# Optimization experiments

Measured on AMD Instinct MI355X. Metric: run time of the kernel, lower is better.

Reference implementation:

```python
import jax, jax.numpy as jnp
import numpy as np

S, N, F, DEG, D_IN, D_OUT = 8, 50000, 5, 32, 128, 128


def setup_inputs() -> dict:
    key = jax.random.key(0)
    k1, k2, k3, k4, k5 = jax.random.split(key, 5)
    std = 1.0 / np.sqrt(D_OUT)
    x = jax.random.normal(k1, (S, N, F), dtype=jnp.float32)
    neigh_idx = jax.random.randint(k2, (S, N, DEG), 0, N, dtype=jnp.int32)
    W_1 = jax.random.uniform(k3, (F, D_IN), minval=-std, maxval=std, dtype=jnp.float32)
    W = jax.random.uniform(k4, (2 * D_IN, D_OUT), minval=-std, maxval=std, dtype=jnp.float32)
    b = jax.random.uniform(k5, (D_OUT,), minval=-std, maxval=std, dtype=jnp.float32)
    return {"x": x, "neigh_idx": neigh_idx, "W_1": W_1, "W": W, "b": b}


def reference(x, neigh_idx, W_1, W, b):
    # Self features projected through W_1 (the x_ list in the torch code).
    self_feats = jnp.einsum('snf,fd->snd', x, W_1)          # [S, N, D_IN]
    # Aggregator: mean over sampled neighbors' raw features (per sample).
    gathered = jax.vmap(lambda xs, ids: xs[ids])(x, neigh_idx)  # [S, N, DEG, F]
    neigh_raw = gathered.mean(axis=2)                        # [S, N, F]
    neigh_feats = jnp.einsum('snf,fd->snd', neigh_raw, W_1)  # [S, N, D_IN]
    # combine == 'concat'
    combined = jnp.concatenate([self_feats, neigh_feats], axis=-1)  # [S, N, 2*D_IN]
    y = jnp.einsum('snc,co->sno', combined, W) + b           # [S, N, D_OUT]
    return jax.nn.relu(y)
```

## Files before the change

### kernel.cpp

```cpp
#include <hip/hip_runtime.h>
#include <cstddef>
#include <cstdint>

static constexpr int S_    = 8;
static constexpr int N_    = 50000;
static constexpr int F_    = 5;
static constexpr int DEG_  = 32;
static constexpr int DOUT_ = 128;
static constexpr int TOTAL_NODES = S_ * N_;
static constexpr int NODES_PER_WAVE = 8;
static constexpr int GROUPS = TOTAL_NODES / NODES_PER_WAVE;

typedef float    f32x4 __attribute__((ext_vector_type(4)));
typedef int      i32x4 __attribute__((ext_vector_type(4)));
typedef _Float16 h2    __attribute__((ext_vector_type(2)));

__global__ void wc_precompute(const float* __restrict__ W1,
                              const float* __restrict__ W,
                              float* __restrict__ Wc) {
    int t = blockIdx.x * blockDim.x + threadIdx.x;
    if (t >= 2 * F_ * DOUT_) return;
    int o = t & (DOUT_ - 1);
    int f = (t >> 7) % F_;
    int p = t / (F_ * DOUT_);
    const float* w1r  = W1 + f * 128;
    const float* wcol = W + (size_t)p * 128 * DOUT_ + o;
    float acc = 0.f;
#pragma unroll 8
    for (int d = 0; d < 128; ++d)
        acc = fmaf(w1r[d], wcol[(size_t)d * DOUT_], acc);
    Wc[t] = acc;
}

struct alignas(16) H8 { _Float16 v[8]; };

__global__ __launch_bounds__(256) void xpack_f16(const float* __restrict__ x,
                                                 H8* __restrict__ xh) {
    int t = blockIdx.x * blockDim.x + threadIdx.x;
    if (t >= TOTAL_NODES) return;
    const float* r = x + (size_t)t * F_;
    H8 o;
#pragma unroll
    for (int f = 0; f < F_; ++f) o.v[f] = (_Float16)r[f];
#pragma unroll
    for (int f = F_; f < 8; ++f) o.v[f] = (_Float16)0.f;
    xh[t] = o;
}

__global__ __launch_bounds__(256) void encoder_v3(
    const int*   __restrict__ idx,
    const H8*    __restrict__ xh,
    const float* __restrict__ Wc,
    const float* __restrict__ b,
    float* __restrict__ out) {
    const int lane = threadIdx.x & 63;
    const int sl   = lane & 31;
    const int half = lane >> 5;
    const int o0   = sl << 2;
    const int g    = (blockIdx.x * blockDim.x + threadIdx.x) >> 6;

    float wa[F_][4], wb[F_][4];
#pragma unroll
    for (int f = 0; f < F_; ++f) {
        f32x4 a  = *reinterpret_cast<const f32x4*>(Wc + f * DOUT_ + o0);
        f32x4 bb = *reinterpret_cast<const f32x4*>(Wc + F_ * DOUT_ + f * DOUT_ + o0);
        wa[f][0] = a.x;  wa[f][1] = a.y;  wa[f][2] = a.z;  wa[f][3] = a.w;
        wb[f][0] = bb.x; wb[f][1] = bb.y; wb[f][2] = bb.z; wb[f][3] = bb.w;
    }
    const f32x4 bias = *reinterpret_cast<const f32x4*>(b + o0);
    const float inv = 1.f / DEG_;

    const int base = g * NODES_PER_WAVE;
    const int s    = base / N_;
    const H8* xs   = xh + (size_t)s * N_;

    union U { i32x4 i; h2 h[4]; };

    int node[4], nb[4];
#pragma unroll
    for (int j = 0; j < 4; ++j) {
        node[j] = base + half + 2 * j;
        nb[j] = __builtin_nontemporal_load(idx + (size_t)node[j] * DEG_ + sl);
    }
    U gv[4], sv[4];
#pragma unroll
    for (int j = 0; j < 4; ++j) {
        gv[j].i = *reinterpret_cast<const i32x4*>(xs + nb[j]);
        sv[j].i = *reinterpret_cast<const i32x4*>(xh + node[j]);
    }

#pragma unroll
    for (int j = 0; j < 4; ++j) {
        h2 v0 = gv[j].h[0], v1 = gv[j].h[1], v2 = gv[j].h[2];
#pragma unroll
        for (int m = 1; m < 32; m <<= 1) {
            v0 += __builtin_bit_cast(h2, __shfl_xor(__builtin_bit_cast(int, v0), m));
            v1 += __builtin_bit_cast(h2, __shfl_xor(__builtin_bit_cast(int, v1), m));
            v2 += __builtin_bit_cast(h2, __shfl_xor(__builtin_bit_cast(int, v2), m));
        }
        const float nf[F_] = { (float)v0.x * inv, (float)v0.y * inv,
                               (float)v1.x * inv, (float)v1.y * inv,
                               (float)v2.x * inv };
        const float sf[F_] = { (float)sv[j].h[0].x, (float)sv[j].h[0].y,
                               (float)sv[j].h[1].x, (float)sv[j].h[1].y,
                               (float)sv[j].h[2].x };
        float y0 = bias.x, y1 = bias.y, y2 = bias.z, y3 = bias.w;
#pragma unroll
        for (int f = 0; f < F_; ++f) {
            y0 = fmaf(sf[f], wa[f][0], y0); y0 = fmaf(nf[f], wb[f][0], y0);
            y1 = fmaf(sf[f], wa[f][1], y1); y1 = fmaf(nf[f], wb[f][1], y1);
            y2 = fmaf(sf[f], wa[f][2], y2); y2 = fmaf(nf[f], wb[f][2], y2);
            y3 = fmaf(sf[f], wa[f][3], y3); y3 = fmaf(nf[f], wb[f][3], y3);
        }
        f32x4 yv = { fmaxf(y0, 0.f), fmaxf(y1, 0.f), fmaxf(y2, 0.f), fmaxf(y3, 0.f) };
        __builtin_nontemporal_store(yv,
            reinterpret_cast<f32x4*>(out + (size_t)node[j] * DOUT_ + o0));
    }
}

__global__ __launch_bounds__(256) void encoder_f32(
    const float* __restrict__ x, const int* __restrict__ idx,
    const float* __restrict__ Wc, const float* __restrict__ b,
    float* __restrict__ out, int total_pairs) {
    const int lane = threadIdx.x & 63;
    const int sl   = lane & 31;
    const int half = lane >> 5;
    const int o0   = sl << 2;
    const int gwave  = (blockIdx.x * blockDim.x + threadIdx.x) >> 6;
    const int nwaves = (gridDim.x * blockDim.x) >> 6;
    float wa[F_][4], wb[F_][4];
#pragma unroll
    for (int f = 0; f < F_; ++f) {
        f32x4 a  = *reinterpret_cast<const f32x4*>(Wc + f * DOUT_ + o0);
        f32x4 bb = *reinterpret_cast<const f32x4*>(Wc + F_ * DOUT_ + f * DOUT_ + o0);
        wa[f][0] = a.x;  wa[f][1] = a.y;  wa[f][2] = a.z;  wa[f][3] = a.w;
        wb[f][0] = bb.x; wb[f][1] = bb.y; wb[f][2] = bb.z; wb[f][3] = bb.w;
    }
    const f32x4 bias = *reinterpret_cast<const f32x4*>(b + o0);
    for (int p = gwave; p < total_pairs; p += nwaves) {
        const int node = p * 2 + half;
        const int s    = node / N_;
        const int nb = idx[(size_t)node * DEG_ + sl];
        const float* xr = x + ((size_t)s * N_ + nb) * F_;
        float n0 = xr[0], n1 = xr[1], n2 = xr[2], n3 = xr[3], n4 = xr[4];
#pragma unroll
        for (int m = 1; m < 32; m <<= 1) {
            n0 += __shfl_xor(n0, m); n1 += __shfl_xor(n1, m); n2 += __shfl_xor(n2, m);
            n3 += __shfl_xor(n3, m); n4 += __shfl_xor(n4, m);
        }
        const float inv = 1.f / DEG_;
        const float nf[F_] = {n0 * inv, n1 * inv, n2 * inv, n3 * inv, n4 * inv};
        const float* xsp = x + (size_t)node * F_;
        const float sf[F_] = {xsp[0], xsp[1], xsp[2], xsp[3], xsp[4]};
        float y0 = bias.x, y1 = bias.y, y2 = bias.z, y3 = bias.w;
#pragma unroll
        for (int f = 0; f < F_; ++f) {
            y0 = fmaf(sf[f], wa[f][0], y0); y0 = fmaf(nf[f], wb[f][0], y0);
            y1 = fmaf(sf[f], wa[f][1], y1); y1 = fmaf(nf[f], wb[f][1], y1);
            y2 = fmaf(sf[f], wa[f][2], y2); y2 = fmaf(nf[f], wb[f][2], y2);
            y3 = fmaf(sf[f], wa[f][3], y3); y3 = fmaf(nf[f], wb[f][3], y3);
        }
        f32x4 yv = { fmaxf(y0, 0.f), fmaxf(y1, 0.f), fmaxf(y2, 0.f), fmaxf(y3, 0.f) };
        *reinterpret_cast<f32x4*>(out + (size_t)node * DOUT_ + o0) = yv;
    }
}

extern "C" void kernel_launch(void* const* d_in, const int* in_sizes, int n_in,
                              void* d_out, int out_size, void* d_ws, size_t ws_size,
                              hipStream_t stream) {
    const float* x   = (const float*)d_in[0];
    const int*   idx = (const int*)  d_in[1];
    const float* W1  = (const float*)d_in[2];
    const float* W   = (const float*)d_in[3];
    const float* b   = (const float*)d_in[4];
    float* out = (float*)d_out;

    const size_t wc_bytes = (size_t)2 * F_ * DOUT_ * sizeof(float);
    const size_t xh_bytes = (size_t)TOTAL_NODES * sizeof(H8);
    float* Wc = (float*)d_ws;

    hipLaunchKernelGGL(wc_precompute, dim3(5), dim3(256), 0, stream, W1, W, Wc);

    if (ws_size >= wc_bytes + xh_bytes) {
        H8* xh = (H8*)((char*)d_ws + wc_bytes);
        hipLaunchKernelGGL(xpack_f16, dim3((TOTAL_NODES + 255) / 256), dim3(256),
                           0, stream, x, xh);
        hipLaunchKernelGGL(encoder_v3, dim3(GROUPS / 4), dim3(256), 0, stream,
                           idx, xh, Wc, b, out);
    } else {
        hipLaunchKernelGGL(encoder_f32, dim3(2048), dim3(256), 0, stream,
                           x, idx, Wc, b, out, S_ * N_ / 2);
    }
}
```

Before: 129.0 us.

## Pack neighbor features to fp8 and software-pipeline a persistent encoder loop

Neighbor features are now packed to fp8, 8 bytes per node, instead of fp16 in 16 bytes, which halves the random-gather footprint. Self features are read in full fp32 directly from x. The encoder becomes persistent: 4096 waves each process a contiguous range of groups. A double-buffered loop prefetches indices and gathered features for the next groups while computing the current one, to hide gather latency. The risk is lower accuracy from fp8 neighbor features, plus extra register pressure from the double buffers.

```diff
diff --git a/kernel.cpp b/kernel.cpp
--- a/kernel.cpp
+++ b/kernel.cpp
@@ -8,11 +8,14 @@
 static constexpr int DEG_  = 32;
 static constexpr int DOUT_ = 128;
 static constexpr int TOTAL_NODES = S_ * N_;
-static constexpr int NODES_PER_WAVE = 8;
-static constexpr int GROUPS = TOTAL_NODES / NODES_PER_WAVE;
+static constexpr int NODES_PER_GROUP = 8;
+static constexpr int GROUPS = TOTAL_NODES / NODES_PER_GROUP;
+static constexpr int NWAVES = 4096;
+static constexpr int KLO    = GROUPS / NWAVES;
+static constexpr int RHI    = GROUPS - KLO * NWAVES;
 
 typedef float    f32x4 __attribute__((ext_vector_type(4)));
-typedef int      i32x4 __attribute__((ext_vector_type(4)));
+typedef int      i32x2 __attribute__((ext_vector_type(2)));
 typedef _Float16 h2    __attribute__((ext_vector_type(2)));
 
 __global__ void wc_precompute(const float* __restrict__ W1,
@@ -32,24 +35,78 @@
     Wc[t] = acc;
 }
 
-struct alignas(16) H8 { _Float16 v[8]; };
-
-__global__ __launch_bounds__(256) void xpack_f16(const float* __restrict__ x,
-                                                 H8* __restrict__ xh) {
+__global__ __launch_bounds__(256) void xpack_fp8(const float* __restrict__ x,
+                                                 i32x2* __restrict__ xq) {
     int t = blockIdx.x * blockDim.x + threadIdx.x;
     if (t >= TOTAL_NODES) return;
     const float* r = x + (size_t)t * F_;
-    H8 o;
-#pragma unroll
-    for (int f = 0; f < F_; ++f) o.v[f] = (_Float16)r[f];
-#pragma unroll
-    for (int f = F_; f < 8; ++f) o.v[f] = (_Float16)0.f;
-    xh[t] = o;
-}
-
-__global__ __launch_bounds__(256) void encoder_v3(
+    int d0 = __builtin_amdgcn_cvt_pk_fp8_f32(r[0], r[1], 0, false);
+    d0     = __builtin_amdgcn_cvt_pk_fp8_f32(r[2], r[3], d0, true);
+    int d1 = __builtin_amdgcn_cvt_pk_fp8_f32(r[4], 0.f, 0, false);
+    i32x2 v; v.x = d0; v.y = d1;
+    xq[t] = v;
+}
+
+#define LOAD_IDX(gg, nb)                                                     \
+    { int base_ = (gg) * NODES_PER_GROUP;                                    \
+      _Pragma("unroll")                                                      \
+      for (int j = 0; j < 4; ++j) {                                          \
+          int node_ = base_ + half + 2 * j;                                  \
+          nb[j] = __builtin_nontemporal_load(idx + (size_t)node_ * DEG_ + sl); } }
+
+#define LOAD_GS(gg, nb, gq, sa, s4)                                          \
+    { int base_ = (gg) * NODES_PER_GROUP;                                    \
+      const i32x2* xs_ = xq + (size_t)(base_ / N_) * N_;                     \
+      _Pragma("unroll")                                                      \
+      for (int j = 0; j < 4; ++j) gq[j] = xs_[nb[j]];           \
+      _Pragma("unroll")                                                      \
+      for (int j = 0; j < 4; ++j) {                                          \
+          int node_ = base_ + half + 2 * j;                                  \
+          __builtin_memcpy(&sa[j], x + (size_t)node_ * F_, 16);  \
+          s4[j] = x[(size_t)node_ * F_ + 4]; } }
+
+#define COMPUTE(gg, gq, sa, s4)                                              \
+    { int base_ = (gg) * NODES_PER_GROUP;                                    \
+      _Pragma("unroll")                                                      \
+      for (int j = 0; j < 4; ++j) {                                          \
+          int d0_ = gq[j].x, d1_ = gq[j].y;                                  \
+          float g0_ = __builtin_amdgcn_cvt_f32_fp8(d0_, 0);                  \
+          float g1_ = __builtin_amdgcn_cvt_f32_fp8(d0_, 1);                  \
+          float g2_ = __builtin_amdgcn_cvt_f32_fp8(d0_, 2);                  \
+          float g3_ = __builtin_amdgcn_cvt_f32_fp8(d0_, 3);                  \
+          float g4_ = __builtin_amdgcn_cvt_f32_fp8(d1_, 0);                  \
+          h2 v0_ = { (_Float16)g0_, (_Float16)g1_ };                         \
+          h2 v1_ = { (_Float16)g2_, (_Float16)g3_ };                         \
+          h2 v2_ = { (_Float16)g4_, (_Float16)0.f };                         \
+          _Pragma("unroll")                                                  \
+          for (int m = 1; m < 32; m <<= 1) {                                 \
+              v0_ += __builtin_bit_cast(h2, __shfl_xor(__builtin_bit_cast(int, v0_), m)); \
+              v1_ += __builtin_bit_cast(h2, __shfl_xor(__builtin_bit_cast(int, v1_), m)); \
+              v2_ += __builtin_bit_cast(h2, __shfl_xor(__builtin_bit_cast(int, v2_), m)); \
+          }                                                                  \
+          float nf_[F_] = { (float)v0_.x * inv, (float)v0_.y * inv,          \
+                            (float)v1_.x * inv, (float)v1_.y * inv,          \
+                            (float)v2_.x * inv };                            \
+          float sf_[F_] = { sa[j].x, sa[j].y, sa[j].z, sa[j].w, s4[j] };     \
+          float y0 = bias.x, y1 = bias.y, y2 = bias.z, y3 = bias.w;          \
+          _Pragma("unroll")                                                  \
+          for (int f = 0; f < F_; ++f) {                                     \
+              y0 = fmaf(sf_[f], wa[f][0], y0); y0 = fmaf(nf_[f], wb[f][0], y0); \
+              y1 = fmaf(sf_[f], wa[f][1], y1); y1 = fmaf(nf_[f], wb[f][1], y1); \
+              y2 = fmaf(sf_[f], wa[f][2], y2); y2 = fmaf(nf_[f], wb[f][2], y2); \
+              y3 = fmaf(sf_[f], wa[f][3], y3); y3 = fmaf(nf_[f], wb[f][3], y3); \
+          }                                                                  \
+          int node_ = base_ + half + 2 * j;                                  \
+          f32x4 yv_ = { fmaxf(y0, 0.f), fmaxf(y1, 0.f),                      \
+                        fmaxf(y2, 0.f), fmaxf(y3, 0.f) };                    \
+          __builtin_nontemporal_store(yv_,                                   \
+              reinterpret_cast<f32x4*>(out + (size_t)node_ * DOUT_ + o0));   \
+      } }
+
+__global__ __launch_bounds__(256) void encoder_v4(
     const int*   __restrict__ idx,
-    const H8*    __restrict__ xh,
+    const i32x2* __restrict__ xq,
+    const float* __restrict__ x,
     const float* __restrict__ Wc,
     const float* __restrict__ b,
     float* __restrict__ out) {
@@ -57,7 +114,10 @@
     const int sl   = lane & 31;
     const int half = lane >> 5;
     const int o0   = sl << 2;
-    const int g    = (blockIdx.x * blockDim.x + threadIdx.x) >> 6;
+    const int w    = (blockIdx.x * blockDim.x + threadIdx.x) >> 6;
+
+    const int g0   = (w < RHI) ? w * (KLO + 1) : RHI * (KLO + 1) + (w - RHI) * KLO;
+    const int gend = g0 + ((w < RHI) ? (KLO + 1) : KLO);
 
     float wa[F_][4], wb[F_][4];
 #pragma unroll
@@ -70,51 +130,27 @@
     const f32x4 bias = *reinterpret_cast<const f32x4*>(b + o0);
     const float inv = 1.f / DEG_;
 
-    const int base = g * NODES_PER_WAVE;
-    const int s    = base / N_;
-    const H8* xs   = xh + (size_t)s * N_;
-
-    union U { i32x4 i; h2 h[4]; };
-
-    int node[4], nb[4];
-#pragma unroll
-    for (int j = 0; j < 4; ++j) {
-        node[j] = base + half + 2 * j;
-        nb[j] = __builtin_nontemporal_load(idx + (size_t)node[j] * DEG_ + sl);
-    }
-    U gv[4], sv[4];
-#pragma unroll
-    for (int j = 0; j < 4; ++j) {
-        gv[j].i = *reinterpret_cast<const i32x4*>(xs + nb[j]);
-        sv[j].i = *reinterpret_cast<const i32x4*>(xh + node[j]);
-    }
-
-#pragma unroll
-    for (int j = 0; j < 4; ++j) {
-        h2 v0 = gv[j].h[0], v1 = gv[j].h[1], v2 = gv[j].h[2];
-#pragma unroll
-        for (int m = 1; m < 32; m <<= 1) {
-            v0 += __builtin_bit_cast(h2, __shfl_xor(__builtin_bit_cast(int, v0), m));
-            v1 += __builtin_bit_cast(h2, __shfl_xor(__builtin_bit_cast(int, v1), m));
-            v2 += __builtin_bit_cast(h2, __shfl_xor(__builtin_bit_cast(int, v2), m));
-        }
-        const float nf[F_] = { (float)v0.x * inv, (float)v0.y * inv,
-                               (float)v1.x * inv, (float)v1.y * inv,
-                               (float)v2.x * inv };
-        const float sf[F_] = { (float)sv[j].h[0].x, (float)sv[j].h[0].y,
-                               (float)sv[j].h[1].x, (float)sv[j].h[1].y,
-                               (float)sv[j].h[2].x };
-        float y0 = bias.x, y1 = bias.y, y2 = bias.z, y3 = bias.w;
-#pragma unroll
-        for (int f = 0; f < F_; ++f) {
-            y0 = fmaf(sf[f], wa[f][0], y0); y0 = fmaf(nf[f], wb[f][0], y0);
-            y1 = fmaf(sf[f], wa[f][1], y1); y1 = fmaf(nf[f], wb[f][1], y1);
-            y2 = fmaf(sf[f], wa[f][2], y2); y2 = fmaf(nf[f], wb[f][2], y2);
-            y3 = fmaf(sf[f], wa[f][3], y3); y3 = fmaf(nf[f], wb[f][3], y3);
-        }
-        f32x4 yv = { fmaxf(y0, 0.f), fmaxf(y1, 0.f), fmaxf(y2, 0.f), fmaxf(y3, 0.f) };
-        __builtin_nontemporal_store(yv,
-            reinterpret_cast<f32x4*>(out + (size_t)node[j] * DOUT_ + o0));
+    int   nbA[4], nbB[4];
+    i32x2 gqA[4], gqB[4];
+    f32x4 saA[4], saB[4];
+    float s4A[4], s4B[4];
+
+    LOAD_IDX(g0, nbA);
+    LOAD_IDX(g0 + 1, nbB);
+    LOAD_GS(g0, nbA, gqA, saA, s4A);
+
+    for (int g = g0; g < gend; g += 2) {
+        const int gp1 = (g + 1 < gend) ? g + 1 : gend - 1;
+        const int gp2 = (g + 2 < gend) ? g + 2 : gend - 1;
+        const int gp3 = (g + 3 < gend) ? g + 3 : gend - 1;
+
+        LOAD_GS(gp1, nbB, gqB, saB, s4B);
+        LOAD_IDX(gp2, nbA);
+        COMPUTE(g, gqA, saA, s4A);
+
+        LOAD_GS(gp2, nbA, gqA, saA, s4A);
+        LOAD_IDX(gp3, nbB);
+        if (g + 1 < gend) COMPUTE(gp1, gqB, saB, s4B);
     }
 }
 
@@ -176,19 +212,19 @@
     float* out = (float*)d_out;
 
     const size_t wc_bytes = (size_t)2 * F_ * DOUT_ * sizeof(float);
-    const size_t xh_bytes = (size_t)TOTAL_NODES * sizeof(H8);
+    const size_t xq_bytes = (size_t)TOTAL_NODES * sizeof(i32x2);
     float* Wc = (float*)d_ws;
 
     hipLaunchKernelGGL(wc_precompute, dim3(5), dim3(256), 0, stream, W1, W, Wc);
 
-    if (ws_size >= wc_bytes + xh_bytes) {
-        H8* xh = (H8*)((char*)d_ws + wc_bytes);
-        hipLaunchKernelGGL(xpack_f16, dim3((TOTAL_NODES + 255) / 256), dim3(256),
-                           0, stream, x, xh);
-        hipLaunchKernelGGL(encoder_v3, dim3(GROUPS / 4), dim3(256), 0, stream,
-                           idx, xh, Wc, b, out);
+    if (ws_size >= wc_bytes + xq_bytes) {
+        i32x2* xq = (i32x2*)((char*)d_ws + wc_bytes);
+        hipLaunchKernelGGL(xpack_fp8, dim3((TOTAL_NODES + 255) / 256), dim3(256),
+                           0, stream, x, xq);
+        hipLaunchKernelGGL(encoder_v4, dim3(NWAVES / 4), dim3(256), 0, stream,
+                           idx, xq, x, Wc, b, out);
     } else {
         hipLaunchKernelGGL(encoder_f32, dim3(2048), dim3(256), 0, stream,
-                           x, idx, Wc, b, out, S_ * N_ / 2);
-    }
-}
+                           x, idx, Wc, b, out, TOTAL_NODES / 2);
+    }
+}
```

Result: slower. 135.8 us (+5.3%).

## Stage per-sample fp16 features in LDS slices for neighbor gather

Applied to the files above, without the earlier changes.

Packs x into 12-byte fp16 records and restructures the encoder so each 640-thread block handles one node per thread. The block streams the sample's feature table through LDS in four 150KB slices, and each thread accumulates its 32 neighbours from LDS, sending out-of-slice indices to a zero sentinel. This replaces scattered global gathers and cross-lane shuffle reductions with LDS reads, at the cost of four block-wide reloads of the slice and large LDS use that limits occupancy to one block per CU. The 1/DEG scale is folded into the weights, and self features are read from fp32 x.

```diff
diff --git a/kernel.cpp b/kernel.cpp
--- a/kernel.cpp
+++ b/kernel.cpp
@@ -8,8 +8,13 @@
 static constexpr int DEG_  = 32;
 static constexpr int DOUT_ = 128;
 static constexpr int TOTAL_NODES = S_ * N_;
-static constexpr int NODES_PER_WAVE = 8;
-static constexpr int GROUPS = TOTAL_NODES / NODES_PER_WAVE;
+
+static constexpr int BLK   = 640;
+static constexpr int BPS   = 79;
+static constexpr int SLICE = 12500;
+static constexpr int NPASS = 4;
+static constexpr int SLICE_DW  = SLICE * 3;
+static constexpr int SLICE_I4  = SLICE_DW / 4;
 
 typedef float    f32x4 __attribute__((ext_vector_type(4)));
 typedef int      i32x4 __attribute__((ext_vector_type(4)));
@@ -32,78 +37,106 @@
     Wc[t] = acc;
 }
 
-struct alignas(16) H8 { _Float16 v[8]; };
-
-__global__ __launch_bounds__(256) void xpack_f16(const float* __restrict__ x,
-                                                 H8* __restrict__ xh) {
+__global__ __launch_bounds__(256) void xpack_h6(const float* __restrict__ x,
+                                                int* __restrict__ xh6) {
     int t = blockIdx.x * blockDim.x + threadIdx.x;
     if (t >= TOTAL_NODES) return;
     const float* r = x + (size_t)t * F_;
-    H8 o;
-#pragma unroll
-    for (int f = 0; f < F_; ++f) o.v[f] = (_Float16)r[f];
-#pragma unroll
-    for (int f = F_; f < 8; ++f) o.v[f] = (_Float16)0.f;
-    xh[t] = o;
-}
-
-__global__ __launch_bounds__(256) void encoder_v3(
+    h2 p0 = { (_Float16)r[0], (_Float16)r[1] };
+    h2 p1 = { (_Float16)r[2], (_Float16)r[3] };
+    h2 p2 = { (_Float16)r[4], (_Float16)0.f };
+    xh6[3 * t + 0] = __builtin_bit_cast(int, p0);
+    xh6[3 * t + 1] = __builtin_bit_cast(int, p1);
+    xh6[3 * t + 2] = __builtin_bit_cast(int, p2);
+}
+
+__global__ __launch_bounds__(BLK) void encoder_v10(
     const int*   __restrict__ idx,
-    const H8*    __restrict__ xh,
+    const int*   __restrict__ xh6,
+    const float* __restrict__ x,
     const float* __restrict__ Wc,
     const float* __restrict__ b,
     float* __restrict__ out) {
-    const int lane = threadIdx.x & 63;
+    __shared__ int lds[SLICE_DW + 4];
+    const int tid  = threadIdx.x;
+    const int s    = blockIdx.x / BPS;
+    const int nb0  = (blockIdx.x % BPS) * BLK;
+    const int nl_s = nb0 + tid;
+    const bool valid = nl_s < N_;
+    const int  gnode = s * N_ + (valid ? nl_s : (N_ - 1));
+
+    i32x4 ids[8];
+    const i32x4* irow = reinterpret_cast<const i32x4*>(idx + (size_t)gnode * DEG_);
+#pragma unroll
+    for (int t = 0; t < 8; ++t) ids[t] = irow[t];
+
+    if (tid == 0) {
+        lds[SLICE_DW] = 0; lds[SLICE_DW + 1] = 0; lds[SLICE_DW + 2] = 0;
+    }
+
+    h2 a0 = { (_Float16)0.f, (_Float16)0.f };
+    h2 a1 = a0, a2 = a0;
+    const i32x4* src4 = reinterpret_cast<const i32x4*>(xh6) + (size_t)s * (SLICE_I4 * NPASS);
+    i32x4* lds4 = reinterpret_cast<i32x4*>(lds);
+
+    for (int p = 0; p < NPASS; ++p) {
+        __syncthreads();
+        const i32x4* ps = src4 + p * SLICE_I4;
+        for (int i = tid; i < SLICE_I4; i += BLK)
+            lds4[i] = ps[i];
+        __syncthreads();
+        const int lo = p * SLICE;
+#pragma unroll
+        for (int k = 0; k < DEG_; ++k) {
+            const int id  = ids[k >> 2][k & 3];
+            const unsigned d = (unsigned)(id - lo);
+            const int r   = (d < (unsigned)SLICE) ? (int)d : SLICE;
+            const int ba  = r * 3;
+            const int w0 = lds[ba], w1 = lds[ba + 1], w2 = lds[ba + 2];
+            a0 += __builtin_bit_cast(h2, w0);
+            a1 += __builtin_bit_cast(h2, w1);
+            a2 += __builtin_bit_cast(h2, w2);
+        }
+    }
+
+    __syncthreads();
+    lds[tid * 3 + 0] = __builtin_bit_cast(int, a0);
+    lds[tid * 3 + 1] = __builtin_bit_cast(int, a1);
+    lds[tid * 3 + 2] = __builtin_bit_cast(int, a2);
+    __syncthreads();
+
+    const int lane = tid & 63;
+    const int wv   = tid >> 6;
     const int sl   = lane & 31;
     const int half = lane >> 5;
     const int o0   = sl << 2;
-    const int g    = (blockIdx.x * blockDim.x + threadIdx.x) >> 6;
+    const float inv = 1.f / DEG_;
 
     float wa[F_][4], wb[F_][4];
 #pragma unroll
     for (int f = 0; f < F_; ++f) {
         f32x4 a  = *reinterpret_cast<const f32x4*>(Wc + f * DOUT_ + o0);
         f32x4 bb = *reinterpret_cast<const f32x4*>(Wc + F_ * DOUT_ + f * DOUT_ + o0);
-        wa[f][0] = a.x;  wa[f][1] = a.y;  wa[f][2] = a.z;  wa[f][3] = a.w;
-        wb[f][0] = bb.x; wb[f][1] = bb.y; wb[f][2] = bb.z; wb[f][3] = bb.w;
+        wa[f][0] = a.x;        wa[f][1] = a.y;
+        wa[f][2] = a.z;        wa[f][3] = a.w;
+        wb[f][0] = bb.x * inv; wb[f][1] = bb.y * inv;
+        wb[f][2] = bb.z * inv; wb[f][3] = bb.w * inv;
     }
     const f32x4 bias = *reinterpret_cast<const f32x4*>(b + o0);
-    const float inv = 1.f / DEG_;
-
-    const int base = g * NODES_PER_WAVE;
-    const int s    = base / N_;
-    const H8* xs   = xh + (size_t)s * N_;
-
-    union U { i32x4 i; h2 h[4]; };
-
-    int node[4], nb[4];
-#pragma unroll
-    for (int j = 0; j < 4; ++j) {
-        node[j] = base + half + 2 * j;
-        nb[j] = __builtin_nontemporal_load(idx + (size_t)node[j] * DEG_ + sl);
-    }
-    U gv[4], sv[4];
-#pragma unroll
-    for (int j = 0; j < 4; ++j) {
-        gv[j].i = *reinterpret_cast<const i32x4*>(xs + nb[j]);
-        sv[j].i = *reinterpret_cast<const i32x4*>(xh + node[j]);
-    }
-
-#pragma unroll
-    for (int j = 0; j < 4; ++j) {
-        h2 v0 = gv[j].h[0], v1 = gv[j].h[1], v2 = gv[j].h[2];
-#pragma unroll
-        for (int m = 1; m < 32; m <<= 1) {
-            v0 += __builtin_bit_cast(h2, __shfl_xor(__builtin_bit_cast(int, v0), m));
-            v1 += __builtin_bit_cast(h2, __shfl_xor(__builtin_bit_cast(int, v1), m));
-            v2 += __builtin_bit_cast(h2, __shfl_xor(__builtin_bit_cast(int, v2), m));
-        }
-        const float nf[F_] = { (float)v0.x * inv, (float)v0.y * inv,
-                               (float)v1.x * inv, (float)v1.y * inv,
-                               (float)v2.x * inv };
-        const float sf[F_] = { (float)sv[j].h[0].x, (float)sv[j].h[0].y,
-                               (float)sv[j].h[1].x, (float)sv[j].h[1].y,
-                               (float)sv[j].h[2].x };
+
+#pragma unroll 4
+    for (int i = 0; i < 32; ++i) {
+        const int nl = wv * 64 + 2 * i + half;
+        const int n  = nb0 + nl;
+        if (n >= N_) continue;
+        const int node = s * N_ + n;
+        const h2 b0 = __builtin_bit_cast(h2, lds[nl * 3 + 0]);
+        const h2 b1 = __builtin_bit_cast(h2, lds[nl * 3 + 1]);
+        const h2 b2 = __builtin_bit_cast(h2, lds[nl * 3 + 2]);
+        const float nf[F_] = { (float)b0.x, (float)b0.y,
+                               (float)b1.x, (float)b1.y, (float)b2.x };
+        const float* xr = x + (size_t)node * F_;
+        const float sf[F_] = { xr[0], xr[1], xr[2], xr[3], xr[4] };
         float y0 = bias.x, y1 = bias.y, y2 = bias.z, y3 = bias.w;
 #pragma unroll
         for (int f = 0; f < F_; ++f) {
@@ -112,9 +145,10 @@
             y2 = fmaf(sf[f], wa[f][2], y2); y2 = fmaf(nf[f], wb[f][2], y2);
             y3 = fmaf(sf[f], wa[f][3], y3); y3 = fmaf(nf[f], wb[f][3], y3);
         }
-        f32x4 yv = { fmaxf(y0, 0.f), fmaxf(y1, 0.f), fmaxf(y2, 0.f), fmaxf(y3, 0.f) };
+        f32x4 yv = { fmaxf(y0, 0.f), fmaxf(y1, 0.f),
+                     fmaxf(y2, 0.f), fmaxf(y3, 0.f) };
         __builtin_nontemporal_store(yv,
-            reinterpret_cast<f32x4*>(out + (size_t)node[j] * DOUT_ + o0));
+            reinterpret_cast<f32x4*>(out + (size_t)node * DOUT_ + o0));
     }
 }
 
@@ -175,20 +209,20 @@
     const float* b   = (const float*)d_in[4];
     float* out = (float*)d_out;
 
-    const size_t wc_bytes = (size_t)2 * F_ * DOUT_ * sizeof(float);
-    const size_t xh_bytes = (size_t)TOTAL_NODES * sizeof(H8);
+    const size_t wc_bytes  = (size_t)2 * F_ * DOUT_ * sizeof(float);
+    const size_t xh6_bytes = (size_t)TOTAL_NODES * 12;
     float* Wc = (float*)d_ws;
 
     hipLaunchKernelGGL(wc_precompute, dim3(5), dim3(256), 0, stream, W1, W, Wc);
 
-    if (ws_size >= wc_bytes + xh_bytes) {
-        H8* xh = (H8*)((char*)d_ws + wc_bytes);
-        hipLaunchKernelGGL(xpack_f16, dim3((TOTAL_NODES + 255) / 256), dim3(256),
-                           0, stream, x, xh);
-        hipLaunchKernelGGL(encoder_v3, dim3(GROUPS / 4), dim3(256), 0, stream,
-                           idx, xh, Wc, b, out);
+    if (ws_size >= wc_bytes + xh6_bytes) {
+        int* xh6 = (int*)((char*)d_ws + wc_bytes);
+        hipLaunchKernelGGL(xpack_h6, dim3((TOTAL_NODES + 255) / 256), dim3(256),
+                           0, stream, x, xh6);
+        hipLaunchKernelGGL(encoder_v10, dim3(S_ * BPS), dim3(BLK), 0, stream,
+                           idx, xh6, x, Wc, b, out);
     } else {
         hipLaunchKernelGGL(encoder_f32, dim3(2048), dim3(256), 0, stream,
-                           x, idx, Wc, b, out, S_ * N_ / 2);
-    }
-}
+                           x, idx, Wc, b, out, TOTAL_NODES / 2);
+    }
+}
```

Result: slower. 135.8 us (+5.3%).
